# Kernel optimization log

Hardware: AMD Instinct MI355X
Metric: run time of the kernel (lower is better)

The kernel has to match this reference:

```python
import jax, jax.numpy as jnp
import numpy as np
from jax import lax

EPS = 1e-8
TAU = 1.0  # step=0 < tau_warmup_steps -> tau = tau_init


def setup_inputs() -> dict:
    key = jax.random.key(0)
    k1, k2 = jax.random.split(key)
    B, D, H, W = 4, 256, 32, 32
    C, K, d = 8, 1024, 32  # n_codebooks, vocab_size, codebook_dim (D = C*d)
    z = jax.random.normal(k1, (B, D, H, W), dtype=jnp.float32)
    cb = jax.random.normal(k2, (C, K, d), dtype=jnp.float32)
    cb = cb / (jnp.linalg.norm(cb, axis=-1, keepdims=True) + 1e-12) * np.sqrt(d).astype(np.float32)
    return {"z": z, "codebooks": cb}


def reference(z, codebooks):
    # Training-mode forward of LGQuantizer (step=0).
    B, D, H, W = z.shape
    C, K, d = codebooks.shape
    # (b d h w) -> (b h w) (c d_sub): chunk along channel dim
    zf = z.transpose(0, 2, 3, 1).reshape(-1, C, d)  # [N, C, d]
    N = zf.shape[0]

    # pairwise squared distances per codebook: [N, C, K]
    z_sq = jnp.sum(zf * zf, axis=-1)                      # [N, C]
    cb_sq = jnp.sum(codebooks * codebooks, axis=-1)       # [C, K]
    cross = jnp.einsum('ncd,ckd->nck', zf, codebooks)     # [N, C, K]
    dists = z_sq[:, :, None] - 2.0 * cross + cb_sq[None, :, :]

    inv_temp = 1.0 / (2.0 * TAU * TAU + EPS)
    logits = -dists * inv_temp
    q = jax.nn.softmax(logits, axis=-1)                   # [N, C, K]

    # soft quantization + straight-through with hard lookup
    z_q = jnp.einsum('nck,ckd->ncd', q, codebooks)        # [N, C, d]
    idx = jnp.argmin(dists, axis=-1)                      # [N, C]
    z_q_hard = codebooks[jnp.arange(C)[None, :], idx]     # [N, C, d]
    z_q_st = z_q + lax.stop_gradient(z_q_hard - z_q)

    quantized = z_q_st.reshape(B, H, W, D).transpose(0, 3, 1, 2)  # [B, D, H, W]
    indices = idx.reshape(B, H, W, C).transpose(0, 3, 1, 2)       # [B, C, H, W]

    # commitment: mse(z_part, q.detach() @ cb.detach()), averaged over codebooks
    commitment = jnp.mean((zf - lax.stop_gradient(z_q)) ** 2)

    log_q = jnp.log(q + EPS)
    neg_ent = jnp.sum(q * log_q, axis=-1)                 # [N, C]
    expected_dist = jnp.mean(jnp.sum(q * dists, axis=-1), axis=0)  # [C]
    kl_uniform = jnp.mean(neg_ent, axis=0) + np.log(K).astype(np.float32)  # [C]
    free_energy = jnp.mean(expected_dist * inv_temp + kl_uniform)

    confidence_loss = jnp.mean(-neg_ent)

    q_bar = jnp.mean(q, axis=0)                           # [C, K]
    balance_loss = jnp.mean(jnp.sum(q_bar * jnp.log(q_bar * K + EPS), axis=-1))

    return (quantized, indices, q, commitment, free_energy,
            confidence_loss, balance_loss, jnp.float32(TAU))
```

## Files before the change

kernel.cpp:

```cpp
#include <hip/hip_runtime.h>

#define WS_A0 0
#define WS_A1 1
#define WS_A2 2
#define WS_QBAR 16
#define WS_CBSQ (WS_QBAR + 8192)
#define WS_IDX  (WS_CBSQ + 8192)

#define OUT_IDX  1048576
#define OUT_Q    1081344
#define OUT_SCAL 34635776

__device__ __forceinline__ float wsum64(float v) {
#pragma unroll
  for (int m = 32; m >= 1; m >>= 1) v += __shfl_xor(v, m, 64);
  return v;
}

__device__ __forceinline__ float uread(float v) {
  return __int_as_float(__builtin_amdgcn_readfirstlane(__float_as_int(v)));
}

#define ZLD 33
__global__ __launch_bounds__(1024, 4)
void k_main(
    const float* __restrict__ z, const float* __restrict__ cb,
    float* __restrict__ out, float* __restrict__ ws_f, int* __restrict__ ws_i) {
  __shared__ __attribute__((aligned(16))) float smem[39040];
  float* cb_lds   = smem;
  float* qsum     = smem + 32768;
  float* cbsq_lds = smem + 33792;
  float* z_lds    = smem + 34816;

  const int c    = blockIdx.x >> 5;
  const int nblk = blockIdx.x & 31;
  const int tid  = threadIdx.x;
  const int lane = tid & 63;
  const int wave = tid >> 6;

  const int bb   = (nblk * 128) >> 10;
  const int hwb  = (nblk * 128) & 1023;

  const float4* cb4 = (const float4*)(cb + (size_t)c * 32768);
  float4* lds4 = (float4*)cb_lds;
#pragma unroll
  for (int i = 0; i < 8; ++i) {
    int idx = i * 1024 + tid;
    int k = idx >> 3, q = idx & 7;
    lds4[(k << 3) + (q ^ (k & 7))] = cb4[idx];
  }
  qsum[tid] = 0.f;
  {
    const float* zbase = z + (((size_t)bb * 256 + c * 32) << 10) + hwb;
#pragma unroll
    for (int i = 0; i < 4; ++i) {
      int idx = i * 1024 + tid;
      int d = idx >> 7, j = idx & 127;
      z_lds[j * ZLD + d] = zbase[(size_t)d * 1024 + j];
    }
  }
  __syncthreads();
  {
    float s = 0.f;
    const int t7 = tid & 7;
#pragma unroll
    for (int q = 0; q < 8; ++q) {
      float4 r4 = lds4[(tid << 3) + (q ^ t7)];
      s = fmaf(r4.x, r4.x, s); s = fmaf(r4.y, r4.y, s);
      s = fmaf(r4.z, r4.z, s); s = fmaf(r4.w, r4.w, s);
    }
    cbsq_lds[tid] = s;
  }
  __syncthreads();

  float* out_q   = out + OUT_Q;
  float* out_idx = out + OUT_IDX;

  float accA0 = 0.f, accA1 = 0.f, accA2 = 0.f;
  const int kl7 = lane & 7;

#pragma unroll 1
  for (int pp = 0; pp < 4; ++pp) {
    const int nl0 = wave * 8 + pp * 2;
    const int nl1 = nl0 + 1;
    const int n0 = nblk * 128 + nl0;
    const int n1 = n0 + 1;

    float zv0[32], zv1[32];
#pragma unroll
    for (int d = 0; d < 32; ++d) {
      zv0[d] = uread(z_lds[nl0 * ZLD + d]);
      zv1[d] = uread(z_lds[nl1 * ZLD + d]);
    }
    float zs0 = 0.f, zs1 = 0.f;
#pragma unroll
    for (int d = 0; d < 32; ++d) {
      zs0 = fmaf(zv0[d], zv0[d], zs0);
      zs1 = fmaf(zv1[d], zv1[d], zs1);
    }

    float S0 = 0.f, S1 = 0.f, es0 = 0.f, es1 = 0.f;
    float zqA0[16], zqA1[16];
#pragma unroll
    for (int i = 0; i < 16; ++i) { zqA0[i] = 0.f; zqA1[i] = 0.f; }

#pragma unroll 1
    for (int jj = 0; jj < 16; ++jj) {
      const int k = jj * 64 + lane;
      const int kbase = k << 3;
      float a0 = 0.f, a1 = 0.f, g0 = 0.f, g1 = 0.f;
#pragma unroll
      for (int qq = 0; qq < 6; ++qq) {
        const int q = (qq + 4) & 7;
        float4 r4 = lds4[kbase + (q ^ kl7)];
        a0 = fmaf(r4.x, zv0[q * 4 + 0], a0);
        a1 = fmaf(r4.y, zv0[q * 4 + 1], a1);
        a0 = fmaf(r4.z, zv0[q * 4 + 2], a0);
        a1 = fmaf(r4.w, zv0[q * 4 + 3], a1);
        g0 = fmaf(r4.x, zv1[q * 4 + 0], g0);
        g1 = fmaf(r4.y, zv1[q * 4 + 1], g1);
        g0 = fmaf(r4.z, zv1[q * 4 + 2], g0);
        g1 = fmaf(r4.w, zv1[q * 4 + 3], g1);
      }
      float4 kq2 = lds4[kbase + (2 ^ kl7)];
      a0 = fmaf(kq2.x, zv0[8], a0);  a1 = fmaf(kq2.y, zv0[9], a1);
      a0 = fmaf(kq2.z, zv0[10], a0); a1 = fmaf(kq2.w, zv0[11], a1);
      g0 = fmaf(kq2.x, zv1[8], g0);  g1 = fmaf(kq2.y, zv1[9], g1);
      g0 = fmaf(kq2.z, zv1[10], g0); g1 = fmaf(kq2.w, zv1[11], g1);
      float4 kq3 = lds4[kbase + (3 ^ kl7)];
      a0 = fmaf(kq3.x, zv0[12], a0); a1 = fmaf(kq3.y, zv0[13], a1);
      a0 = fmaf(kq3.z, zv0[14], a0); a1 = fmaf(kq3.w, zv0[15], a1);
      g0 = fmaf(kq3.x, zv1[12], g0); g1 = fmaf(kq3.y, zv1[13], g1);
      g0 = fmaf(kq3.z, zv1[14], g0); g1 = fmaf(kq3.w, zv1[15], g1);

      float cq = cbsq_lds[k];
      float s0 = (a0 + a1) - 0.5f * cq;
      float s1 = (g0 + g1) - 0.5f * cq;
      float ev0 = __expf(s0), ev1 = __expf(s1);
      S0 += ev0;  S1 += ev1;
      es0 = fmaf(ev0, s0, es0);
      es1 = fmaf(ev1, s1, es1);
#pragma unroll
      for (int q = 0; q < 2; ++q) {
        float4 r4 = lds4[kbase + (q ^ kl7)];
        zqA0[q * 4 + 0] = fmaf(ev0, r4.x, zqA0[q * 4 + 0]);
        zqA0[q * 4 + 1] = fmaf(ev0, r4.y, zqA0[q * 4 + 1]);
        zqA0[q * 4 + 2] = fmaf(ev0, r4.z, zqA0[q * 4 + 2]);
        zqA0[q * 4 + 3] = fmaf(ev0, r4.w, zqA0[q * 4 + 3]);
        zqA1[q * 4 + 0] = fmaf(ev1, r4.x, zqA1[q * 4 + 0]);
        zqA1[q * 4 + 1] = fmaf(ev1, r4.y, zqA1[q * 4 + 1]);
        zqA1[q * 4 + 2] = fmaf(ev1, r4.z, zqA1[q * 4 + 2]);
        zqA1[q * 4 + 3] = fmaf(ev1, r4.w, zqA1[q * 4 + 3]);
      }
      zqA0[8]  = fmaf(ev0, kq2.x, zqA0[8]);  zqA0[9]  = fmaf(ev0, kq2.y, zqA0[9]);
      zqA0[10] = fmaf(ev0, kq2.z, zqA0[10]); zqA0[11] = fmaf(ev0, kq2.w, zqA0[11]);
      zqA1[8]  = fmaf(ev1, kq2.x, zqA1[8]);  zqA1[9]  = fmaf(ev1, kq2.y, zqA1[9]);
      zqA1[10] = fmaf(ev1, kq2.z, zqA1[10]); zqA1[11] = fmaf(ev1, kq2.w, zqA1[11]);
      zqA0[12] = fmaf(ev0, kq3.x, zqA0[12]); zqA0[13] = fmaf(ev0, kq3.y, zqA0[13]);
      zqA0[14] = fmaf(ev0, kq3.z, zqA0[14]); zqA0[15] = fmaf(ev0, kq3.w, zqA0[15]);
      zqA1[12] = fmaf(ev1, kq3.x, zqA1[12]); zqA1[13] = fmaf(ev1, kq3.y, zqA1[13]);
      zqA1[14] = fmaf(ev1, kq3.z, zqA1[14]); zqA1[15] = fmaf(ev1, kq3.w, zqA1[15]);
    }

    float St0 = wsum64(S0), St1 = wsum64(S1);
    float rS0 = 1.f / St0, rS1 = 1.f / St1;
    float est0 = wsum64(es0), est1 = wsum64(es1);

    accA1 += (zs0 - 2.f * est0 * rS0) + (zs1 - 2.f * est1 * rS1);
    accA2 += (est0 * rS0 - __logf(St0)) + (est1 * rS1 - __logf(St1));

    {
#pragma unroll
      for (int t = 0; t < 4; ++t) {
        const int half = 8 >> t;
        const int up = (lane >> (5 - t)) & 1;
#pragma unroll
        for (int i = 0; i < half; ++i) {
          float sa0 = up ? zqA0[i] : zqA0[i + half];
          float ka0 = up ? zqA0[i + half] : zqA0[i];
          zqA0[i] = ka0 + __shfl_xor(sa0, 32 >> t, 64);
          float sa1 = up ? zqA1[i] : zqA1[i + half];
          float ka1 = up ? zqA1[i + half] : zqA1[i];
          zqA1[i] = ka1 + __shfl_xor(sa1, 32 >> t, 64);
        }
      }
      zqA0[0] += __shfl_xor(zqA0[0], 2, 64);
      zqA0[0] += __shfl_xor(zqA0[0], 1, 64);
      zqA1[0] += __shfl_xor(zqA1[0], 2, 64);
      zqA1[0] += __shfl_xor(zqA1[0], 1, 64);
      const int ddA = (lane >> 2) & 15;
      float dA0 = z_lds[nl0 * ZLD + ddA] - zqA0[0] * rS0;
      float dA1 = z_lds[nl1 * ZLD + ddA] - zqA1[0] * rS1;
      accA0 += 0.25f * wsum64(dA0 * dA0 + dA1 * dA1);
    }

    float sm0 = -INFINITY, sm1 = -INFINITY;
    int km0 = 0, km1 = 0;
    float zqB0[16], zqB1[16];
#pragma unroll
    for (int i = 0; i < 16; ++i) { zqB0[i] = 0.f; zqB1[i] = 0.f; }
    float* qp0 = out_q + ((size_t)n0 * 8 + c) * 1024;
    float* qp1 = out_q + ((size_t)n1 * 8 + c) * 1024;

#pragma unroll 1
    for (int jj = 0; jj < 16; ++jj) {
      const int k = jj * 64 + lane;
      const int kbase = k << 3;
      float a0 = 0.f, a1 = 0.f, g0 = 0.f, g1 = 0.f;
#pragma unroll
      for (int q = 0; q < 6; ++q) {
        float4 r4 = lds4[kbase + (q ^ kl7)];
        a0 = fmaf(r4.x, zv0[q * 4 + 0], a0);
        a1 = fmaf(r4.y, zv0[q * 4 + 1], a1);
        a0 = fmaf(r4.z, zv0[q * 4 + 2], a0);
        a1 = fmaf(r4.w, zv0[q * 4 + 3], a1);
        g0 = fmaf(r4.x, zv1[q * 4 + 0], g0);
        g1 = fmaf(r4.y, zv1[q * 4 + 1], g1);
        g0 = fmaf(r4.z, zv1[q * 4 + 2], g0);
        g1 = fmaf(r4.w, zv1[q * 4 + 3], g1);
      }
      float4 kq6 = lds4[kbase + (6 ^ kl7)];
      a0 = fmaf(kq6.x, zv0[24], a0); a1 = fmaf(kq6.y, zv0[25], a1);
      a0 = fmaf(kq6.z, zv0[26], a0); a1 = fmaf(kq6.w, zv0[27], a1);
      g0 = fmaf(kq6.x, zv1[24], g0); g1 = fmaf(kq6.y, zv1[25], g1);
      g0 = fmaf(kq6.z, zv1[26], g0); g1 = fmaf(kq6.w, zv1[27], g1);
      float4 kq7 = lds4[kbase + (7 ^ kl7)];
      a0 = fmaf(kq7.x, zv0[28], a0); a1 = fmaf(kq7.y, zv0[29], a1);
      a0 = fmaf(kq7.z, zv0[30], a0); a1 = fmaf(kq7.w, zv0[31], a1);
      g0 = fmaf(kq7.x, zv1[28], g0); g1 = fmaf(kq7.y, zv1[29], g1);
      g0 = fmaf(kq7.z, zv1[30], g0); g1 = fmaf(kq7.w, zv1[31], g1);

      float cq = cbsq_lds[k];
      float s0 = (a0 + a1) - 0.5f * cq;
      float s1 = (g0 + g1) - 0.5f * cq;
      if (s0 > sm0) { sm0 = s0; km0 = k; }
      if (s1 > sm1) { sm1 = s1; km1 = k; }
      float qv0 = __expf(s0) * rS0;
      float qv1 = __expf(s1) * rS1;
      __builtin_nontemporal_store(qv0, qp0 + jj * 64 + lane);
      __builtin_nontemporal_store(qv1, qp1 + jj * 64 + lane);
      atomicAdd(&qsum[jj * 64 + lane], qv0 + qv1);
#pragma unroll
      for (int q = 4; q < 6; ++q) {
        float4 r4 = lds4[kbase + (q ^ kl7)];
        const int i0 = (q - 4) * 4;
        zqB0[i0 + 0] = fmaf(qv0, r4.x, zqB0[i0 + 0]);
        zqB0[i0 + 1] = fmaf(qv0, r4.y, zqB0[i0 + 1]);
        zqB0[i0 + 2] = fmaf(qv0, r4.z, zqB0[i0 + 2]);
        zqB0[i0 + 3] = fmaf(qv0, r4.w, zqB0[i0 + 3]);
        zqB1[i0 + 0] = fmaf(qv1, r4.x, zqB1[i0 + 0]);
        zqB1[i0 + 1] = fmaf(qv1, r4.y, zqB1[i0 + 1]);
        zqB1[i0 + 2] = fmaf(qv1, r4.z, zqB1[i0 + 2]);
        zqB1[i0 + 3] = fmaf(qv1, r4.w, zqB1[i0 + 3]);
      }
      zqB0[8]  = fmaf(qv0, kq6.x, zqB0[8]);  zqB0[9]  = fmaf(qv0, kq6.y, zqB0[9]);
      zqB0[10] = fmaf(qv0, kq6.z, zqB0[10]); zqB0[11] = fmaf(qv0, kq6.w, zqB0[11]);
      zqB1[8]  = fmaf(qv1, kq6.x, zqB1[8]);  zqB1[9]  = fmaf(qv1, kq6.y, zqB1[9]);
      zqB1[10] = fmaf(qv1, kq6.z, zqB1[10]); zqB1[11] = fmaf(qv1, kq6.w, zqB1[11]);
      zqB0[12] = fmaf(qv0, kq7.x, zqB0[12]); zqB0[13] = fmaf(qv0, kq7.y, zqB0[13]);
      zqB0[14] = fmaf(qv0, kq7.z, zqB0[14]); zqB0[15] = fmaf(qv0, kq7.w, zqB0[15]);
      zqB1[12] = fmaf(qv1, kq7.x, zqB1[12]); zqB1[13] = fmaf(qv1, kq7.y, zqB1[13]);
      zqB1[14] = fmaf(qv1, kq7.z, zqB1[14]); zqB1[15] = fmaf(qv1, kq7.w, zqB1[15]);
    }

#pragma unroll
    for (int m = 32; m >= 1; m >>= 1) {
      float so = __shfl_xor(sm0, m, 64); int ko = __shfl_xor(km0, m, 64);
      if (so > sm0 || (so == sm0 && ko < km0)) { sm0 = so; km0 = ko; }
      float sp = __shfl_xor(sm1, m, 64); int kp = __shfl_xor(km1, m, 64);
      if (sp > sm1 || (sp == sm1 && kp < km1)) { sm1 = sp; km1 = kp; }
    }
    if (lane == 0) {
      out_idx[(size_t)bb * 8192 + c * 1024 + hwb + nl0] = (float)km0;
      ws_i[WS_IDX + n0 * 8 + c] = km0;
      out_idx[(size_t)bb * 8192 + c * 1024 + hwb + nl1] = (float)km1;
      ws_i[WS_IDX + n1 * 8 + c] = km1;
    }

#pragma unroll
    for (int t = 0; t < 4; ++t) {
      const int half = 8 >> t;
      const int up = (lane >> (5 - t)) & 1;
#pragma unroll
      for (int i = 0; i < half; ++i) {
        float sa0 = up ? zqB0[i] : zqB0[i + half];
        float ka0 = up ? zqB0[i + half] : zqB0[i];
        zqB0[i] = ka0 + __shfl_xor(sa0, 32 >> t, 64);
        float sa1 = up ? zqB1[i] : zqB1[i + half];
        float ka1 = up ? zqB1[i + half] : zqB1[i];
        zqB1[i] = ka1 + __shfl_xor(sa1, 32 >> t, 64);
      }
    }
    zqB0[0] += __shfl_xor(zqB0[0], 2, 64);
    zqB0[0] += __shfl_xor(zqB0[0], 1, 64);
    zqB1[0] += __shfl_xor(zqB1[0], 2, 64);
    zqB1[0] += __shfl_xor(zqB1[0], 1, 64);
    const int ddB = (lane >> 2) & 15;
    float dB0 = z_lds[nl0 * ZLD + 16 + ddB] - zqB0[0];
    float dB1 = z_lds[nl1 * ZLD + 16 + ddB] - zqB1[0];
    accA0 += 0.25f * wsum64(dB0 * dB0 + dB1 * dB1);
  }

  if (lane == 0) {
    atomicAdd(&ws_f[WS_A0], accA0);
    atomicAdd(&ws_f[WS_A1], accA1);
    atomicAdd(&ws_f[WS_A2], accA2);
  }

  __syncthreads();
  atomicAdd(&ws_f[WS_QBAR + c * 1024 + tid], qsum[tid]);
}

__global__ __launch_bounds__(256) void k_hard(const float* __restrict__ cb,
                                              const int* __restrict__ ws_i,
                                              float* __restrict__ out0,
                                              const float* __restrict__ ws_f,
                                              float* __restrict__ out_s) {
  int o = blockIdx.x * 256 + threadIdx.x;
  int b  = o >> 18;
  int r  = o & 262143;
  int ch = r >> 10;
  int hw = r & 1023;
  int c = ch >> 5, dd = ch & 31;
  int n = (b << 10) + hw;
  int k = ws_i[WS_IDX + n * 8 + c];
  out0[o] = cb[((size_t)(c << 10) + k) * 32 + dd];

  if (blockIdx.x == 0) {
    __shared__ float red[256];
    int tid = threadIdx.x;
    float bal = 0.f;
    for (int i = tid; i < 8192; i += 256) {
      float qb = ws_f[WS_QBAR + i] * (1.0f / 4096.0f);
      bal += qb * __logf(qb * 1024.0f + 1e-8f);
    }
    red[tid] = bal;
    __syncthreads();
    for (int s = 128; s > 0; s >>= 1) {
      if (tid < s) red[tid] += red[tid + s];
      __syncthreads();
    }
    if (tid == 0) {
      float A0 = ws_f[WS_A0], A1 = ws_f[WS_A1], A2 = ws_f[WS_A2];
      out_s[0] = A0 * (1.0f / 1048576.0f);
      out_s[1] = (0.5f * A1 + A2) * (1.0f / 32768.0f) + 6.93147180559945f;
      out_s[2] = -A2 * (1.0f / 32768.0f);
      out_s[3] = red[0] * 0.125f;
      out_s[4] = 1.0f;
    }
  }
}

extern "C" void kernel_launch(void* const* d_in, const int* in_sizes, int n_in,
                              void* d_out, int out_size, void* d_ws, size_t ws_size,
                              hipStream_t stream) {
  (void)in_sizes; (void)n_in; (void)out_size; (void)ws_size;
  const float* z  = (const float*)d_in[0];
  const float* cb = (const float*)d_in[1];
  float* out  = (float*)d_out;
  float* ws_f = (float*)d_ws;
  int*   ws_i = (int*)d_ws;

  hipMemsetAsync(d_ws, 0, (WS_QBAR + 8192) * sizeof(float), stream);
  k_main <<<256, 1024, 0, stream>>>(z, cb, out, ws_f, ws_i);
  k_hard <<<4096, 256, 0, stream>>>(cb, ws_i, out, ws_f, out + OUT_SCAL);
}
```

Before: 448.4 us.

## Reuse codebook LDS loads, defer commitment reduction, vectorize hard-lookup stores

In the second pass of the main kernel, codebook quads 4 and 5 are now loaded once and reused for both the distance dot product and the soft-quantization accumulation, removing two LDS reads per iteration. The cb-squared read is hoisted to the top of each loop, and the per-point wave reduction of the commitment error is replaced by per-lane accumulation with a single wave sum at the end. The hard-lookup kernel now has each thread gather four hw-consecutive outputs and write them as one float4, with a quarter of the blocks. Together these target LDS bandwidth, shuffle overhead and store instruction count, at the cost of slightly different floating-point summation order and more registers held live.

```diff
diff --git a/kernel.cpp b/kernel.cpp
--- a/kernel.cpp
+++ b/kernel.cpp
@@ -76,7 +76,8 @@
   float* out_q   = out + OUT_Q;
   float* out_idx = out + OUT_IDX;
 
-  float accA0 = 0.f, accA1 = 0.f, accA2 = 0.f;
+  float accA1 = 0.f, accA2 = 0.f;
+  float a0loc = 0.f;
   const int kl7 = lane & 7;
 
 #pragma unroll 1
@@ -108,6 +109,7 @@
     for (int jj = 0; jj < 16; ++jj) {
       const int k = jj * 64 + lane;
       const int kbase = k << 3;
+      float cq = cbsq_lds[k];
       float a0 = 0.f, a1 = 0.f, g0 = 0.f, g1 = 0.f;
 #pragma unroll
       for (int qq = 0; qq < 6; ++qq) {
@@ -133,7 +135,6 @@
       g0 = fmaf(kq3.x, zv1[12], g0); g1 = fmaf(kq3.y, zv1[13], g1);
       g0 = fmaf(kq3.z, zv1[14], g0); g1 = fmaf(kq3.w, zv1[15], g1);
 
-      float cq = cbsq_lds[k];
       float s0 = (a0 + a1) - 0.5f * cq;
       float s1 = (g0 + g1) - 0.5f * cq;
       float ev0 = __expf(s0), ev1 = __expf(s1);
@@ -191,7 +192,7 @@
       const int ddA = (lane >> 2) & 15;
       float dA0 = z_lds[nl0 * ZLD + ddA] - zqA0[0] * rS0;
       float dA1 = z_lds[nl1 * ZLD + ddA] - zqA1[0] * rS1;
-      accA0 += 0.25f * wsum64(dA0 * dA0 + dA1 * dA1);
+      a0loc += dA0 * dA0 + dA1 * dA1;
     }
 
     float sm0 = -INFINITY, sm1 = -INFINITY;
@@ -206,9 +207,10 @@
     for (int jj = 0; jj < 16; ++jj) {
       const int k = jj * 64 + lane;
       const int kbase = k << 3;
+      float cq = cbsq_lds[k];
       float a0 = 0.f, a1 = 0.f, g0 = 0.f, g1 = 0.f;
 #pragma unroll
-      for (int q = 0; q < 6; ++q) {
+      for (int q = 0; q < 4; ++q) {
         float4 r4 = lds4[kbase + (q ^ kl7)];
         a0 = fmaf(r4.x, zv0[q * 4 + 0], a0);
         a1 = fmaf(r4.y, zv0[q * 4 + 1], a1);
@@ -219,6 +221,16 @@
         g0 = fmaf(r4.z, zv1[q * 4 + 2], g0);
         g1 = fmaf(r4.w, zv1[q * 4 + 3], g1);
       }
+      float4 kq4 = lds4[kbase + (4 ^ kl7)];
+      a0 = fmaf(kq4.x, zv0[16], a0); a1 = fmaf(kq4.y, zv0[17], a1);
+      a0 = fmaf(kq4.z, zv0[18], a0); a1 = fmaf(kq4.w, zv0[19], a1);
+      g0 = fmaf(kq4.x, zv1[16], g0); g1 = fmaf(kq4.y, zv1[17], g1);
+      g0 = fmaf(kq4.z, zv1[18], g0); g1 = fmaf(kq4.w, zv1[19], g1);
+      float4 kq5 = lds4[kbase + (5 ^ kl7)];
+      a0 = fmaf(kq5.x, zv0[20], a0); a1 = fmaf(kq5.y, zv0[21], a1);
+      a0 = fmaf(kq5.z, zv0[22], a0); a1 = fmaf(kq5.w, zv0[23], a1);
+      g0 = fmaf(kq5.x, zv1[20], g0); g1 = fmaf(kq5.y, zv1[21], g1);
+      g0 = fmaf(kq5.z, zv1[22], g0); g1 = fmaf(kq5.w, zv1[23], g1);
       float4 kq6 = lds4[kbase + (6 ^ kl7)];
       a0 = fmaf(kq6.x, zv0[24], a0); a1 = fmaf(kq6.y, zv0[25], a1);
       a0 = fmaf(kq6.z, zv0[26], a0); a1 = fmaf(kq6.w, zv0[27], a1);
@@ -230,7 +242,6 @@
       g0 = fmaf(kq7.x, zv1[28], g0); g1 = fmaf(kq7.y, zv1[29], g1);
       g0 = fmaf(kq7.z, zv1[30], g0); g1 = fmaf(kq7.w, zv1[31], g1);
 
-      float cq = cbsq_lds[k];
       float s0 = (a0 + a1) - 0.5f * cq;
       float s1 = (g0 + g1) - 0.5f * cq;
       if (s0 > sm0) { sm0 = s0; km0 = k; }
@@ -240,19 +251,14 @@
       __builtin_nontemporal_store(qv0, qp0 + jj * 64 + lane);
       __builtin_nontemporal_store(qv1, qp1 + jj * 64 + lane);
       atomicAdd(&qsum[jj * 64 + lane], qv0 + qv1);
-#pragma unroll
-      for (int q = 4; q < 6; ++q) {
-        float4 r4 = lds4[kbase + (q ^ kl7)];
-        const int i0 = (q - 4) * 4;
-        zqB0[i0 + 0] = fmaf(qv0, r4.x, zqB0[i0 + 0]);
-        zqB0[i0 + 1] = fmaf(qv0, r4.y, zqB0[i0 + 1]);
-        zqB0[i0 + 2] = fmaf(qv0, r4.z, zqB0[i0 + 2]);
-        zqB0[i0 + 3] = fmaf(qv0, r4.w, zqB0[i0 + 3]);
-        zqB1[i0 + 0] = fmaf(qv1, r4.x, zqB1[i0 + 0]);
-        zqB1[i0 + 1] = fmaf(qv1, r4.y, zqB1[i0 + 1]);
-        zqB1[i0 + 2] = fmaf(qv1, r4.z, zqB1[i0 + 2]);
-        zqB1[i0 + 3] = fmaf(qv1, r4.w, zqB1[i0 + 3]);
-      }
+      zqB0[0]  = fmaf(qv0, kq4.x, zqB0[0]);  zqB0[1]  = fmaf(qv0, kq4.y, zqB0[1]);
+      zqB0[2]  = fmaf(qv0, kq4.z, zqB0[2]);  zqB0[3]  = fmaf(qv0, kq4.w, zqB0[3]);
+      zqB1[0]  = fmaf(qv1, kq4.x, zqB1[0]);  zqB1[1]  = fmaf(qv1, kq4.y, zqB1[1]);
+      zqB1[2]  = fmaf(qv1, kq4.z, zqB1[2]);  zqB1[3]  = fmaf(qv1, kq4.w, zqB1[3]);
+      zqB0[4]  = fmaf(qv0, kq5.x, zqB0[4]);  zqB0[5]  = fmaf(qv0, kq5.y, zqB0[5]);
+      zqB0[6]  = fmaf(qv0, kq5.z, zqB0[6]);  zqB0[7]  = fmaf(qv0, kq5.w, zqB0[7]);
+      zqB1[4]  = fmaf(qv1, kq5.x, zqB1[4]);  zqB1[5]  = fmaf(qv1, kq5.y, zqB1[5]);
+      zqB1[6]  = fmaf(qv1, kq5.z, zqB1[6]);  zqB1[7]  = fmaf(qv1, kq5.w, zqB1[7]);
       zqB0[8]  = fmaf(qv0, kq6.x, zqB0[8]);  zqB0[9]  = fmaf(qv0, kq6.y, zqB0[9]);
       zqB0[10] = fmaf(qv0, kq6.z, zqB0[10]); zqB0[11] = fmaf(qv0, kq6.w, zqB0[11]);
       zqB1[8]  = fmaf(qv1, kq6.x, zqB1[8]);  zqB1[9]  = fmaf(qv1, kq6.y, zqB1[9]);
@@ -298,9 +304,10 @@
     const int ddB = (lane >> 2) & 15;
     float dB0 = z_lds[nl0 * ZLD + 16 + ddB] - zqB0[0];
     float dB1 = z_lds[nl1 * ZLD + 16 + ddB] - zqB1[0];
-    accA0 += 0.25f * wsum64(dB0 * dB0 + dB1 * dB1);
-  }
-
+    a0loc += dB0 * dB0 + dB1 * dB1;
+  }
+
+  float accA0 = 0.25f * wsum64(a0loc);
   if (lane == 0) {
     atomicAdd(&ws_f[WS_A0], accA0);
     atomicAdd(&ws_f[WS_A1], accA1);
@@ -316,15 +323,22 @@
                                               float* __restrict__ out0,
                                               const float* __restrict__ ws_f,
                                               float* __restrict__ out_s) {
-  int o = blockIdx.x * 256 + threadIdx.x;
+  int o4 = blockIdx.x * 256 + threadIdx.x;
+  int o  = o4 << 2;
   int b  = o >> 18;
   int r  = o & 262143;
   int ch = r >> 10;
   int hw = r & 1023;
   int c = ch >> 5, dd = ch & 31;
   int n = (b << 10) + hw;
-  int k = ws_i[WS_IDX + n * 8 + c];
-  out0[o] = cb[((size_t)(c << 10) + k) * 32 + dd];
+  const int* ip = ws_i + WS_IDX + n * 8 + c;
+  const float* cbc = cb + ((size_t)c << 15) + dd;
+  float4 v;
+  v.x = cbc[(size_t)ip[0]  * 32];
+  v.y = cbc[(size_t)ip[8]  * 32];
+  v.z = cbc[(size_t)ip[16] * 32];
+  v.w = cbc[(size_t)ip[24] * 32];
+  *(float4*)(out0 + o) = v;
 
   if (blockIdx.x == 0) {
     __shared__ float red[256];
@@ -363,5 +377,5 @@
 
   hipMemsetAsync(d_ws, 0, (WS_QBAR + 8192) * sizeof(float), stream);
   k_main <<<256, 1024, 0, stream>>>(z, cb, out, ws_f, ws_i);
-  k_hard <<<4096, 256, 0, stream>>>(cb, ws_i, out, ws_f, out + OUT_SCAL);
-}
+  k_hard <<<1024, 256, 0, stream>>>(cb, ws_i, out, ws_f, out + OUT_SCAL);
+}
```

New measurement: 436.4 us. 1.03x faster.
